# Optimization experiments

Hardware: AMD Instinct MI355X
Metric: run time of the kernel (lower is better)

## Reference

```python
import jax, jax.numpy as jnp
import numpy as np

B, S, T = 1024, 1024, 32  # batch, seq_len, num_tags


def setup_inputs() -> dict:
    key = jax.random.key(0)
    k1, k2, k3, k4 = jax.random.split(key, 4)
    logits = jax.random.normal(k1, (B, S, T), dtype=jnp.float32)
    transitions = jax.random.normal(k2, (T, T), dtype=jnp.float32)
    tags = jax.random.randint(k3, (B, S), 0, T)
    lengths = jax.random.randint(k4, (B,), 1, S + 1)
    return {"logits": logits, "transitions": transitions, "tags": tags, "lengths": lengths}


def _forward_alg(logits, transitions):
    # viterbi_0 = logits[:, 0, :]; then for t>=1:
    # v_next[b, j] = logsumexp_i(v[b, i] + trans[i, j]) + logits[b, t, j]
    v0 = logits[:, 0, :]  # (B, T)
    emits = jnp.swapaxes(logits[:, 1:, :], 0, 1)  # (S-1, B, T)

    def step(v, emit_t):
        v_next = jax.nn.logsumexp(v[:, :, None] + transitions[None, :, :], axis=1) + emit_t
        return v_next, None

    v_final, _ = jax.lax.scan(step, v0, emits)
    return jax.nn.logsumexp(v_final, axis=1)  # (B,)


def _score_sentence(logits, transitions, tags, lengths):
    # emission scores of gold tags, masked to t < length (note: original ignores
    # lengths in the forward algorithm but uses them here, faithfully reproduced)
    emit = jnp.take_along_axis(logits, tags[:, :, None], axis=2)[..., 0]  # (B, S)
    pos = jnp.arange(S)
    emit_mask = (pos[None, :] < lengths[:, None]).astype(logits.dtype)
    score = jnp.sum(emit * emit_mask, axis=1)
    # transition scores trans[tags[t-1], tags[t]] for 1 <= t < length
    trans_sc = transitions[tags[:, :-1], tags[:, 1:]]  # (B, S-1)
    trans_mask = (pos[None, 1:] < lengths[:, None]).astype(logits.dtype)
    score = score + jnp.sum(trans_sc * trans_mask, axis=1)
    return score  # (B,)


def reference(logits, transitions, tags, lengths):
    log_z = _forward_alg(logits, transitions)
    gold = _score_sentence(logits, transitions, tags, lengths)
    return jnp.mean(log_z - gold)
```

## Files before the change

kernel.cpp:

```cpp
#include <hip/hip_runtime.h>

#define NB 1024
#define NS 1024
#define NT 32
#define L2E 1.44269504088896340736f
#define LN2 0.69314718055994530942f

typedef short        bfrag  __attribute__((ext_vector_type(8)));
typedef float        cfrag  __attribute__((ext_vector_type(16)));
typedef __bf16       bf16x2 __attribute__((ext_vector_type(2)));
typedef float        f32x8  __attribute__((ext_vector_type(8)));
typedef float        f32x4  __attribute__((ext_vector_type(4)));
typedef float        f32x2  __attribute__((ext_vector_type(2)));
typedef unsigned int u32;
typedef unsigned int u32x2v __attribute__((ext_vector_type(2)));
typedef unsigned int u32x4  __attribute__((ext_vector_type(4)));

__device__ __forceinline__ float fexp2(float x){ return __builtin_amdgcn_exp2f(x); }
__device__ __forceinline__ float flog2(float x){ return __builtin_amdgcn_logf(x); }

__device__ __forceinline__ u32 pkbf_rne(float a, float b){
    f32x2 t; t.x = a; t.y = b;
    return __builtin_bit_cast(u32, __builtin_convertvector(t, bf16x2));
}
__device__ __forceinline__ u32 pkbf_t(float a, float b){
    return __builtin_amdgcn_perm(__builtin_bit_cast(u32, b),
                                 __builtin_bit_cast(u32, a), 0x07060302u);
}
__device__ __forceinline__ bfrag mk_afrag(f32x8 v){
    u32x4 r;
    r[0] = pkbf_rne(v[0], v[1]); r[1] = pkbf_rne(v[2], v[3]);
    r[2] = pkbf_rne(v[4], v[5]); r[3] = pkbf_rne(v[6], v[7]);
    return __builtin_bit_cast(bfrag, r);
}

#if __has_builtin(__builtin_amdgcn_permlane32_swap)
#define HAVE_PLSWAP 1
#else
#define HAVE_PLSWAP 0
#endif

__device__ __forceinline__ void half_swap(u32 &x, u32 &y, int h){
#if HAVE_PLSWAP
    u32x2v r = __builtin_amdgcn_permlane32_swap(x, y, false, false);
    x = r[0]; y = r[1];
#else
    u32 X  = __shfl_xor(h ? x : y, 32, 64);
    u32 nx = h ? X : x;
    u32 ny = h ? y : X;
    x = nx; y = ny;
#endif
}

template<int N> struct ic { static constexpr int value = N; };
union accu { cfrag c; f32x2 p[8]; };
union q4u  { f32x4 v; f32x2 p[2]; };

__global__ __launch_bounds__(256, 8) void crf_chunk(
    const float* __restrict__ logits, const float* __restrict__ trans,
    u32* __restrict__ wmat, float* __restrict__ woff)
{
    __shared__ __align__(16) float dscall[4 * 512];

    const int tid = threadIdx.x;
    const int wv  = tid >> 6, lt = tid & 63;
    const int m   = lt & 31,  h  = lt >> 5;
    const int bc  = blockIdx.x * 4 + wv;
    const int b   = bc >> 3,  c  = bc & 7;
    float* dsc = dscall + wv * 512;

    const float* base = logits + (size_t)b * NS * NT;

    f32x8 Et0, Et1;
    #pragma unroll
    for (int j = 0; j < 8; j++){
        Et0[j] = fexp2(L2E * trans[(     8*h + j)*NT + m]);
        Et1[j] = fexp2(L2E * trans[(16 + 8*h + j)*NT + m]);
    }
    const bfrag A0f = mk_afrag(Et0);
    const bfrag A1f = mk_afrag(Et1);

    u32x4 B0v, B1v;
    #pragma unroll
    for (int d = 0; d < 4; d++){
        int k0 = 8*h + 2*d;      u32 v = 0;
        if (k0     == m) v |= 0x3F80u;
        if (k0 + 1 == m) v |= 0x3F800000u;
        B0v[d] = v;
        int k1 = 16 + 8*h + 2*d; v = 0;
        if (k1     == m) v |= 0x3F80u;
        if (k1 + 1 == m) v |= 0x3F800000u;
        B1v[d] = v;
    }

    cfrag zacc;
    #pragma unroll
    for (int q = 0; q < 16; q++) zacc[q] = 0.0f;

    int   offi = 0;
    float exf  = 0.0f;
    const int tbeg = c*128 + 1;

    float eA[4], eB[4];

    auto issue = [&](float (&e)[4], int k){
        const int t0 = tbeg + k*8 + 4*h;
        #pragma unroll
        for (int i = 0; i < 4; i++){
            int t = t0 + i; t = t > (NS-1) ? (NS-1) : t;
            e[i] = base[t*NT + m];
        }
    };
    auto commit = [&](float (&e)[4], int k){
        float* sp = dsc + (k & 1)*256 + (4*h)*32 + m;
        float a0 = (h == 0) ? -exf : 0.0f;
        sp[0]    = fexp2(fmaf(L2E, e[0], a0));
        sp[32]   = fexp2(L2E * e[1]);
        sp[64]   = fexp2(L2E * e[2]);
        sp[96]   = fexp2(L2E * e[3]);
    };

    auto exref = [&](float ref)->int{
        u32 xb = __builtin_bit_cast(u32, ref);
        u32 xf = __builtin_amdgcn_readfirstlane(xb);
        int ex = (int)((xf >> 23) & 0xFFu) - 127;
        return ex < -120 ? -120 : (ex > 120 ? 120 : ex);
    };

    auto procN = [&](int k, bool defer, auto nstc){
        constexpr int NST = decltype(nstc)::value;
        const float* db = dsc + (k & 1)*256 + 4*h;
        #pragma unroll
        for (int i = 0; i < NST; i++){
            accu acc;
            acc.c = __builtin_amdgcn_mfma_f32_32x32x16_bf16(
                        A0f, __builtin_bit_cast(bfrag, B0v), zacc, 0, 0, 0);
            acc.c = __builtin_amdgcn_mfma_f32_32x32x16_bf16(
                        A1f, __builtin_bit_cast(bfrag, B1v), acc.c, 0, 0, 0);

            q4u d0, d1, d2, d3;
            d0.v = *(const f32x4*)(db + i*32 +  0);
            d1.v = *(const f32x4*)(db + i*32 +  8);
            d2.v = *(const f32x4*)(db + i*32 + 16);
            d3.v = *(const f32x4*)(db + i*32 + 24);
            acc.p[0] *= d0.p[0]; acc.p[1] *= d0.p[1];
            acc.p[2] *= d1.p[0]; acc.p[3] *= d1.p[1];
            acc.p[4] *= d2.p[0]; acc.p[5] *= d2.p[1];
            acc.p[6] *= d3.p[0]; acc.p[7] *= d3.p[1];

            if (i == 3){
                int ex = exref(fmaxf(acc.c[0], acc.c[8]));
                offi += ex;
                f32x2 s2;
                s2.x = s2.y = __builtin_bit_cast(float, (u32)(127 - ex) << 23);
                #pragma unroll
                for (int q = 0; q < 8; q++) acc.p[q] *= s2;
            }
            if (i == 7 && defer){
                int ex = exref(fmaxf(acc.c[0], acc.c[8]));
                offi += ex;
                exf = (float)ex;
            }

            u32 P0 = pkbf_t(acc.c[0],  acc.c[1]),  P1 = pkbf_t(acc.c[2],  acc.c[3]);
            u32 P2 = pkbf_t(acc.c[4],  acc.c[5]),  P3 = pkbf_t(acc.c[6],  acc.c[7]);
            u32 P4 = pkbf_t(acc.c[8],  acc.c[9]),  P5 = pkbf_t(acc.c[10], acc.c[11]);
            u32 P6 = pkbf_t(acc.c[12], acc.c[13]), P7 = pkbf_t(acc.c[14], acc.c[15]);
            half_swap(P0, P2, h); half_swap(P1, P3, h);
            half_swap(P4, P6, h); half_swap(P5, P7, h);
            B0v[0]=P0; B0v[1]=P1; B0v[2]=P2; B0v[3]=P3;
            B1v[0]=P4; B1v[1]=P5; B1v[2]=P6; B1v[3]=P7;
        }
    };

    issue(eA, 0); commit(eA, 0);
    #pragma unroll 1
    for (int k = 0; k < 14; k += 2){
        issue(eB, k + 1);
        procN(k, true, ic<8>{});
        commit(eB, k + 1);
        issue(eA, k + 2);
        procN(k + 1, true, ic<8>{});
        commit(eA, k + 2);
    }
    issue(eB, 15);
    procN(14, true, ic<8>{});
    commit(eB, 15);
    if (c != 7) procN(15, false, ic<8>{});
    else        procN(15, false, ic<7>{});

    const size_t mb = (size_t)bc * 512;
    #pragma unroll
    for (int d = 0; d < 4; d++){
        wmat[mb + d*64 + lt]     = B0v[d];
        wmat[mb + (4+d)*64 + lt] = B1v[d];
    }
    if (lt == 0) woff[bc] = (float)offi;
}

__global__ __launch_bounds__(64) void crf_combine(
    const float* __restrict__ logits, const float* __restrict__ trans,
    const int* __restrict__ tags, const int* __restrict__ lens,
    const u32* __restrict__ wmat, const float* __restrict__ woff,
    float* __restrict__ out)
{
    __shared__ __align__(16) float ldsT[NT*NT];
    __shared__ __align__(16) int   ldsTag[NS];
    __shared__ __align__(16) float ldsU[NT];

    const int tid = threadIdx.x;
    const int m   = tid & 31;
    const int b   = blockIdx.x;
    const int len = lens[b];
    const float* lgb = logits + (size_t)b * NS * NT;

    #pragma unroll
    for (int i = 0; i < 16; i++) ldsT[tid + i*64] = trans[tid + i*64];
    const int4* tg4 = (const int4*)(tags + b*NS);
    #pragma unroll
    for (int i = 0; i < 4; i++) ((int4*)ldsTag)[tid + i*64] = tg4[tid + i*64];
    __syncthreads();

    float g = 0.0f;
    #pragma unroll
    for (int it = 0; it < 16; it++){
        int t = tid + it*64;
        if (t < len){
            int tg = ldsTag[t];
            g += lgb[t*NT + tg];
            if (t >= 1) g += ldsT[ldsTag[t-1]*NT + tg];
        }
    }

    float v = fexp2(L2E * lgb[m]);
    float voff = 0.0f;

    const int n  = m;
    const int f  = n >> 4;
    const int hh = (n >> 3) & 1;
    const int di = f*4 + ((n >> 1) & 3);

    for (int cc = 0; cc < 8; cc++){
        const int bcn = b*8 + cc;
        float offc = woff[bcn];
        float w = flog2(v) + offc;
        float mw = w;
        #pragma unroll
        for (int d = 1; d <= 16; d <<= 1) mw = fmaxf(mw, __shfl_xor(mw, d, 64));
        float u = fexp2(w - mw);
        if (tid < 32) ldsU[m] = u;
        __syncthreads();

        const uint4* mp = (const uint4*)(wmat + (size_t)bcn*512 + di*64 + hh*32);
        float acc = 0.0f;
        #pragma unroll
        for (int qq = 0; qq < 8; qq++){
            uint4  md = mp[qq];
            float4 uu = ((const float4*)ldsU)[qq];
            float e0 = __builtin_bit_cast(float, (n&1) ? (md.x & 0xFFFF0000u) : (md.x << 16));
            float e1 = __builtin_bit_cast(float, (n&1) ? (md.y & 0xFFFF0000u) : (md.y << 16));
            float e2 = __builtin_bit_cast(float, (n&1) ? (md.z & 0xFFFF0000u) : (md.z << 16));
            float e3 = __builtin_bit_cast(float, (n&1) ? (md.w & 0xFFFF0000u) : (md.w << 16));
            acc = fmaf(e0, uu.x, acc);
            acc = fmaf(e1, uu.y, acc);
            acc = fmaf(e2, uu.z, acc);
            acc = fmaf(e3, uu.w, acc);
        }
        v = acc;
        voff += mw;
        __syncthreads();
    }

    float s = v;
    #pragma unroll
    for (int d = 1; d <= 16; d <<= 1) s += __shfl_xor(s, d, 64);
    #pragma unroll
    for (int d = 1; d <= 32; d <<= 1) g += __shfl_xor(g, d, 64);
    if (tid == 0){
        float logz = LN2 * (voff + flog2(s));
        atomicAdd(out, (logz - g) * (1.0f / (float)NB));
    }
}

extern "C" void kernel_launch(void* const* d_in, const int* in_sizes, int n_in,
                              void* d_out, int out_size, void* d_ws, size_t ws_size,
                              hipStream_t stream) {
    const float* logits = (const float*)d_in[0];
    const float* trans  = (const float*)d_in[1];
    const int*   tags   = (const int*)d_in[2];
    const int*   lens   = (const int*)d_in[3];

    u32*   wmat = (u32*)d_ws;
    float* woff = (float*)(wmat + 8192*512);

    hipMemsetAsync(d_out, 0, sizeof(float), stream);
    crf_chunk  <<<2048, 256, 0, stream>>>(logits, trans, wmat, woff);
    crf_combine<<<1024, 64, 0, stream>>>(logits, trans, tags, lens, wmat, woff,
                                         (float*)d_out);
}
```

Before: 262.9 us.

## Split gold-score into separate wide kernel and double-buffer combine matrix loads

Moves the gold-path score computation out of the 64-thread combine kernel into its own 256-thread-per-batch kernel that reads contiguous tag groups, and makes the combine kernel prefetch the next chunk's matrix rows into registers while processing the current one, with all offsets loaded up front. The aim is to take the latency-bound gather off the serial combine chain and hide global-load latency across chunks. In exchange it adds an extra kernel launch and more register pressure in the combine kernel.

```diff
diff --git a/kernel.cpp b/kernel.cpp
--- a/kernel.cpp
+++ b/kernel.cpp
@@ -198,41 +198,67 @@
     if (lt == 0) woff[bc] = (float)offi;
 }
 
-__global__ __launch_bounds__(64) void crf_combine(
+__global__ __launch_bounds__(256) void crf_gold(
     const float* __restrict__ logits, const float* __restrict__ trans,
     const int* __restrict__ tags, const int* __restrict__ lens,
-    const u32* __restrict__ wmat, const float* __restrict__ woff,
     float* __restrict__ out)
 {
     __shared__ __align__(16) float ldsT[NT*NT];
     __shared__ __align__(16) int   ldsTag[NS];
+    __shared__ float red[4];
+
+    const int tid = threadIdx.x;
+    const int b   = blockIdx.x;
+    const int len = lens[b];
+    const float* lgb = logits + (size_t)b * NS * NT;
+
+    ((float4*)ldsT)[tid]  = ((const float4*)trans)[tid];
+    ((int4*)ldsTag)[tid]  = ((const int4*)(tags + (size_t)b * NS))[tid];
+    __syncthreads();
+
+    const int t0 = tid * 4;
+    int4 tgv = ((const int4*)ldsTag)[tid];
+    int  prv = ldsTag[tid == 0 ? 0 : t0 - 1];
+    int tgs[5] = {prv, tgv.x, tgv.y, tgv.z, tgv.w};
+
+    float g = 0.0f;
+    #pragma unroll
+    for (int i = 0; i < 4; i++){
+        int t = t0 + i;
+        if (t < len){
+            float e  = lgb[t*NT + tgs[i+1]];
+            float tr = (t >= 1) ? ldsT[tgs[i]*NT + tgs[i+1]] : 0.0f;
+            g += e + tr;
+        }
+    }
+
+    #pragma unroll
+    for (int d = 1; d < 64; d <<= 1) g += __shfl_xor(g, d, 64);
+    if ((tid & 63) == 0) red[tid >> 6] = g;
+    __syncthreads();
+    if (tid == 0){
+        float gs = red[0] + red[1] + red[2] + red[3];
+        atomicAdd(out, -gs * (1.0f / (float)NB));
+    }
+}
+
+__global__ __launch_bounds__(64) void crf_combine(
+    const float* __restrict__ logits,
+    const u32* __restrict__ wmat, const float* __restrict__ woff,
+    float* __restrict__ out)
+{
     __shared__ __align__(16) float ldsU[NT];
 
     const int tid = threadIdx.x;
     const int m   = tid & 31;
     const int b   = blockIdx.x;
-    const int len = lens[b];
     const float* lgb = logits + (size_t)b * NS * NT;
 
-    #pragma unroll
-    for (int i = 0; i < 16; i++) ldsT[tid + i*64] = trans[tid + i*64];
-    const int4* tg4 = (const int4*)(tags + b*NS);
-    #pragma unroll
-    for (int i = 0; i < 4; i++) ((int4*)ldsTag)[tid + i*64] = tg4[tid + i*64];
-    __syncthreads();
-
-    float g = 0.0f;
-    #pragma unroll
-    for (int it = 0; it < 16; it++){
-        int t = tid + it*64;
-        if (t < len){
-            int tg = ldsTag[t];
-            g += lgb[t*NT + tg];
-            if (t >= 1) g += ldsT[ldsTag[t-1]*NT + tg];
-        }
-    }
-
-    float v = fexp2(L2E * lgb[m]);
+    float offs[8];
+    #pragma unroll
+    for (int cc = 0; cc < 8; cc++) offs[cc] = woff[b*8 + cc];
+
+    float v    = fexp2(L2E * lgb[m]);
     float voff = 0.0f;
 
     const int n  = m;
@@ -240,10 +266,22 @@
     const int hh = (n >> 3) & 1;
     const int di = f*4 + ((n >> 1) & 3);
 
+    auto ldrow = [&](int cc, uint4 (&md)[8]){
+        const uint4* mp = (const uint4*)(wmat + (size_t)(b*8 + cc)*512 + di*64 + hh*32);
+        #pragma unroll
+        for (int qq = 0; qq < 8; qq++) md[qq] = mp[qq];
+    };
+
+    uint4 mdA[8], mdB[8];
+    ldrow(0, mdA);
+
+    #pragma unroll
     for (int cc = 0; cc < 8; cc++){
-        const int bcn = b*8 + cc;
-        float offc = woff[bcn];
-        float w = flog2(v) + offc;
+        uint4 (&cur)[8] = (cc & 1) ? mdB : mdA;
+        uint4 (&nxt)[8] = (cc & 1) ? mdA : mdB;
+        if (cc < 7) ldrow(cc + 1, nxt);
+
+        float w  = flog2(v) + offs[cc];
         float mw = w;
         #pragma unroll
         for (int d = 1; d <= 16; d <<= 1) mw = fmaxf(mw, __shfl_xor(mw, d, 64));
@@ -251,11 +289,10 @@
         if (tid < 32) ldsU[m] = u;
         __syncthreads();
 
-        const uint4* mp = (const uint4*)(wmat + (size_t)bcn*512 + di*64 + hh*32);
         float acc = 0.0f;
         #pragma unroll
         for (int qq = 0; qq < 8; qq++){
-            uint4  md = mp[qq];
+            uint4  md = cur[qq];
             float4 uu = ((const float4*)ldsU)[qq];
             float e0 = __builtin_bit_cast(float, (n&1) ? (md.x & 0xFFFF0000u) : (md.x << 16));
             float e1 = __builtin_bit_cast(float, (n&1) ? (md.y & 0xFFFF0000u) : (md.y << 16));
@@ -274,11 +311,9 @@
     float s = v;
     #pragma unroll
     for (int d = 1; d <= 16; d <<= 1) s += __shfl_xor(s, d, 64);
-    #pragma unroll
-    for (int d = 1; d <= 32; d <<= 1) g += __shfl_xor(g, d, 64);
     if (tid == 0){
         float logz = LN2 * (voff + flog2(s));
-        atomicAdd(out, (logz - g) * (1.0f / (float)NB));
+        atomicAdd(out, logz * (1.0f / (float)NB));
     }
 }
 
@@ -295,6 +330,6 @@
 
     hipMemsetAsync(d_out, 0, sizeof(float), stream);
     crf_chunk  <<<2048, 256, 0, stream>>>(logits, trans, wmat, woff);
-    crf_combine<<<1024, 64, 0, stream>>>(logits, trans, tags, lens, wmat, woff,
-                                         (float*)d_out);
-}
+    crf_gold   <<<1024, 256, 0, stream>>>(logits, trans, tags, lens, (float*)d_out);
+    crf_combine<<<1024,  64, 0, stream>>>(logits, wmat, woff, (float*)d_out);
+}
```

New measurement: 278.6 us. 1.06x slower.
